# Performance work log

Hardware: AMD Instinct MI355X
Metric: run time of the kernel (lower is better)

The kernel has to match this reference:

```python
import jax, jax.numpy as jnp
import numpy as np

B, S, D, H, L, MLP, WIN = 4, 1024, 256, 8, 2, 1024, 64
HD = D // H
NEG = -1e9  # emulates -inf additive mask; exp underflows to exact 0

_idx = jnp.arange(S)
BAND = jnp.where(jnp.abs(_idx[:, None] - _idx[None, :]) <= WIN, 0.0, NEG).astype(jnp.float32)


def setup_inputs() -> dict:
    key = jax.random.key(0)
    ks = iter(jax.random.split(key, 16))
    r = lambda shape, s=0.02: jax.random.normal(next(ks), shape, dtype=jnp.float32) * s
    return {
        "x": jax.random.normal(next(ks), (B, S, D), dtype=jnp.float32),
        "scale": jnp.ones((1,), jnp.float32) * (D ** -0.5),
        "Win_a": r((L, 3 * D, D)), "bin_a": jnp.zeros((L, 3 * D), jnp.float32),
        "Wout_a": r((L, D, D)), "bout_a": jnp.zeros((L, D), jnp.float32),
        "Win_e": r((L, 3 * D, D)), "bin_e": jnp.zeros((L, 3 * D), jnp.float32),
        "Wout_e": r((L, D, D)), "bout_e": jnp.zeros((L, D), jnp.float32),
        "ln1_g": jnp.ones((L, D), jnp.float32), "ln1_b": jnp.zeros((L, D), jnp.float32),
        "ln2_g": jnp.ones((L, D), jnp.float32), "ln2_b": jnp.zeros((L, D), jnp.float32),
        "W1": r((L, MLP, D)), "b1": jnp.zeros((L, MLP), jnp.float32),
        "W2": r((L, D, MLP)), "b2": jnp.zeros((L, D), jnp.float32),
        "lnf_g": jnp.ones((D,), jnp.float32), "lnf_b": jnp.zeros((D,), jnp.float32),
    }


def _layernorm(x, g, b, eps=1e-5):
    m = jnp.mean(x, axis=-1, keepdims=True)
    v = jnp.mean(jnp.square(x - m), axis=-1, keepdims=True)
    return (x - m) * jax.lax.rsqrt(v + eps) * g + b


def _mha(x, Win, bin_, Wout, bout, mask=None):
    # torch nn.MultiheadAttention (batch_first=True), dropout=0
    b, s, _ = x.shape
    qkv = x @ Win.T + bin_                       # (b, s, 3D)
    q, k, v = jnp.split(qkv, 3, axis=-1)
    split = lambda t: t.reshape(b, s, H, HD).transpose(0, 2, 1, 3)  # (b, H, s, HD)
    q, k, v = split(q), split(k), split(v)
    scores = jnp.einsum('bhqd,bhkd->bhqk', q, k) / np.float32(np.sqrt(HD))
    if mask is not None:
        scores = scores + mask
    attn = jax.nn.softmax(scores, axis=-1)
    out = jnp.einsum('bhqk,bhkd->bhqd', attn, v).transpose(0, 2, 1, 3).reshape(b, s, D)
    return out @ Wout.T + bout


def reference(x, scale, Win_a, bin_a, Wout_a, bout_a, Win_e, bin_e, Wout_e, bout_e,
              ln1_g, ln1_b, ln2_g, ln2_b, W1, b1, W2, b2, lnf_g, lnf_b):
    # ScaledSinusoidalPositionalEncoding returns arange(S)*scale, shape (S,1)
    pos = jnp.arange(S, dtype=jnp.float32) * scale[0]   # (S,)
    x = x + pos[:, None]                                 # broadcast (B,S,D)+(S,1)
    for l in range(L):
        xi = _mha(x, Win_a[l], bin_a[l], Wout_a[l], bout_a[l])
        x = _layernorm(x + xi, ln1_g[l], ln1_b[l])
        xe = _mha(x, Win_e[l], bin_e[l], Wout_e[l], bout_e[l], mask=BAND)
        attended = _layernorm(x + xe, ln2_g[l], ln2_b[l])
        h = jax.nn.gelu(attended @ W1[l].T + b1[l], approximate=False)
        x = attended + h @ W2[l].T + b2[l]
    return _layernorm(x, lnf_g, lnf_b)
```

## Files before the change

kernel.cpp:

```cpp
#include <hip/hip_runtime.h>
#include <math.h>

#define BB 4
#define SS 1024
#define DD 256
#define HH 8
#define HD 32
#define D3 768
#define MLP 1024
#define NTOK (BB * SS)
#define NSEG 4

typedef __attribute__((ext_vector_type(8))) short short8;
typedef __attribute__((ext_vector_type(4))) float f32x4;

__device__ __forceinline__ unsigned short f2bfu(float f) {
    union { float f; unsigned i; } u; u.f = f;
    unsigned r = u.i + 0x7fffu + ((u.i >> 16) & 1u);
    return (unsigned short)(r >> 16);
}
__device__ __forceinline__ float bfu2f(unsigned short h) {
    union { unsigned i; float f; } u; u.i = ((unsigned)h) << 16; return u.f;
}

#define W_TOT 2097152
#define WL0   196608
#define WBLK  (W_TOT / 256)
#define PBLK  (NTOK * DD / 256)
__global__ __launch_bounds__(256) void prep_kernel(
    const float* __restrict__ a0, const float* __restrict__ a1,
    const float* __restrict__ a2, const float* __restrict__ a3,
    const float* __restrict__ a4, const float* __restrict__ a5,
    unsigned short* __restrict__ out, unsigned short* __restrict__ out_lo,
    const float* __restrict__ x, const float* __restrict__ scale,
    float* __restrict__ xf, unsigned short* __restrict__ xh,
    unsigned short* __restrict__ xl)
{
    if (blockIdx.x < WBLK) {
        int i = blockIdx.x * 256 + threadIdx.x;
        const float* s; int off;
        if      (i <  393216) { s = a0; off = 0;       }
        else if (i <  524288) { s = a1; off = 393216;  }
        else if (i <  917504) { s = a2; off = 524288;  }
        else if (i < 1048576) { s = a3; off = 917504;  }
        else if (i < 1572864) { s = a4; off = 1048576; }
        else                  { s = a5; off = 1572864; }
        float v = s[i - off];
        unsigned short h = f2bfu(v);
        out[i] = h;
        if (i < WL0) out_lo[i] = f2bfu(v - bfu2f(h));
    } else {
        int i = (blockIdx.x - WBLK) * 256 + threadIdx.x;
        int s = (i >> 8) & (SS - 1);
        float v = x[i] + (float)s * scale[0];
        xf[i] = v;
        unsigned short h = f2bfu(v);
        xh[i] = h;
        xl[i] = f2bfu(v - bfu2f(h));
    }
}

__device__ __forceinline__ size_t vt_index(int row, int col512) {
    int b = row >> 10, s = row & (SS - 1);
    int h = col512 >> 5, d = col512 & (HD - 1);
    return (((size_t)b * HH + h) * HD + d) * SS + s;
}

#define LDP 40
__global__ __launch_bounds__(256) void gemm_mfma(
    const unsigned short* __restrict__ A, const unsigned short* __restrict__ W,
    const float* __restrict__ bias, const float* __restrict__ resid,
    float* __restrict__ outf, unsigned short* __restrict__ outb,
    unsigned short* __restrict__ vth,
    int M, int N, int K, int act)
{
    __shared__ __align__(16) unsigned short As[64 * LDP];
    __shared__ __align__(16) unsigned short Bs[128 * LDP];
    const int t = threadIdx.x;
    const int lane = t & 63, wave = t >> 6;
    const int wr = wave >> 1, wc = wave & 1;
    const int m0 = blockIdx.y * 64, n0 = blockIdx.x * 128;
    const int sr = t >> 2;
    const int sc = (t & 3) * 8;

    const unsigned short* Ag = A + (size_t)(m0 + sr) * K + sc;
    const unsigned short* Wg = W + (size_t)(n0 + sr) * K + sc;

    f32x4 acc[2][4];
    #pragma unroll
    for (int i = 0; i < 2; i++)
        #pragma unroll
        for (int j = 0; j < 4; j++)
            acc[i][j] = (f32x4){0.f, 0.f, 0.f, 0.f};

    const int lm = lane & 15, lk = (lane >> 4) * 8;

    uint4 a0 = *(const uint4*)(Ag);
    uint4 b0 = *(const uint4*)(Wg);
    uint4 b1 = *(const uint4*)(Wg + (size_t)64 * K);

    for (int k0 = 0; k0 < K; k0 += 32) {
        __syncthreads();
        *(uint4*)&As[sr * LDP + sc]        = a0;
        *(uint4*)&Bs[sr * LDP + sc]        = b0;
        *(uint4*)&Bs[(sr + 64) * LDP + sc] = b1;
        __syncthreads();
        if (k0 + 32 < K) {
            a0 = *(const uint4*)(Ag + k0 + 32);
            b0 = *(const uint4*)(Wg + k0 + 32);
            b1 = *(const uint4*)(Wg + (size_t)64 * K + k0 + 32);
        }

        short8 af[2], bf[4];
        #pragma unroll
        for (int i = 0; i < 2; i++)
            af[i] = *(const short8*)&As[(wr * 32 + i * 16 + lm) * LDP + lk];
        #pragma unroll
        for (int j = 0; j < 4; j++)
            bf[j] = *(const short8*)&Bs[(wc * 64 + j * 16 + lm) * LDP + lk];
        #pragma unroll
        for (int i = 0; i < 2; i++)
            #pragma unroll
            for (int j = 0; j < 4; j++)
                acc[i][j] = __builtin_amdgcn_mfma_f32_16x16x32_bf16(
                    af[i], bf[j], acc[i][j], 0, 0, 0);
    }

    const int lq = lane >> 4;
    #pragma unroll
    for (int j = 0; j < 4; j++) {
        int col = n0 + wc * 64 + j * 16 + lm;
        float bv = bias[col];
        #pragma unroll
        for (int i = 0; i < 2; i++) {
            #pragma unroll
            for (int r = 0; r < 4; r++) {
                int row = m0 + wr * 32 + i * 16 + lq * 4 + r;
                float v = acc[i][j][r] + bv;
                if (act) v = 0.5f * v * (1.0f + erff(v * 0.70710678118654752f));
                if (vth && col >= 2 * DD) {
                    vth[vt_index(row, col - 2 * DD)] = f2bfu(v);
                } else {
                    size_t idx = (size_t)row * N + col;
                    if (resid) v += resid[idx];
                    if (outf) outf[idx] = v;
                    if (outb) outb[idx] = f2bfu(v);
                }
            }
        }
    }
}

template<bool COMBINE, bool DOLN>
__global__ __launch_bounds__(256) void gemm_ln(
    const unsigned short* __restrict__ A,
    const float* __restrict__ Of, const float2* __restrict__ Ml,
    const unsigned short* __restrict__ W, const float* __restrict__ bias,
    const float* __restrict__ resid,
    const float* __restrict__ g, const float* __restrict__ bt,
    float* __restrict__ outf, unsigned short* __restrict__ outb, int K)
{
    __shared__ __align__(16) unsigned short As[16 * LDP];
    __shared__ __align__(16) unsigned short Bs[256 * LDP];
    __shared__ float rsum[4][16];
    __shared__ float rsum2[4][16];
    const int t = threadIdx.x;
    const int lane = t & 63, wave = t >> 6;
    const int m0 = blockIdx.x * 16;
    const int sr = t >> 2;
    const int sc = (t & 3) * 8;
    const int arow = t >> 2;
    const int acol = (t & 3) * 8;

    const unsigned short* Wg = W + (size_t)sr * K + sc;

    f32x4 acc[4];
    #pragma unroll
    for (int j = 0; j < 4; j++) acc[j] = (f32x4){0.f, 0.f, 0.f, 0.f};

    const int lm = lane & 15, lk = (lane >> 4) * 8;
    const int quad = lane >> 4;

    for (int k0 = 0; k0 < K; k0 += 32) {
        unsigned short ab[8];
        const bool aload = (t < 64);
        if (aload) {
            const int token = m0 + arow;
            if (COMBINE) {
                const int h = (k0 + acol) >> 5;
                float2 ml[NSEG];
                float M = -1e30f;
                #pragma unroll
                for (int s = 0; s < NSEG; s++) {
                    ml[s] = Ml[((size_t)s * NTOK + token) * HH + h];
                    M = fmaxf(M, ml[s].x);
                }
                float wgt[NSEG]; float denom = 0.f;
                #pragma unroll
                for (int s = 0; s < NSEG; s++) {
                    wgt[s] = __expf(ml[s].x - M);
                    denom += ml[s].y * wgt[s];
                }
                const float inv = 1.0f / denom;
                float a8[8] = {};
                #pragma unroll
                for (int s = 0; s < NSEG; s++) {
                    const float* p = Of + ((size_t)s * NTOK + token) * DD + k0 + acol;
                    float4 x0 = *(const float4*)p;
                    float4 x1 = *(const float4*)(p + 4);
                    a8[0] += x0.x * wgt[s]; a8[1] += x0.y * wgt[s];
                    a8[2] += x0.z * wgt[s]; a8[3] += x0.w * wgt[s];
                    a8[4] += x1.x * wgt[s]; a8[5] += x1.y * wgt[s];
                    a8[6] += x1.z * wgt[s]; a8[7] += x1.w * wgt[s];
                }
                #pragma unroll
                for (int c = 0; c < 8; c++) ab[c] = f2bfu(a8[c] * inv);
            } else {
                uint4 av = *(const uint4*)(A + (size_t)(m0 + arow) * K + k0 + acol);
                *(uint4*)ab = av;
            }
        }
        uint4 b0 = *(const uint4*)(Wg + k0);
        uint4 b1 = *(const uint4*)(Wg + (size_t)64 * K + k0);
        uint4 b2 = *(const uint4*)(Wg + (size_t)128 * K + k0);
        uint4 b3 = *(const uint4*)(Wg + (size_t)192 * K + k0);
        __syncthreads();
        if (aload) *(uint4*)&As[arow * LDP + acol] = *(uint4*)ab;
        *(uint4*)&Bs[sr * LDP + sc]         = b0;
        *(uint4*)&Bs[(sr + 64) * LDP + sc]  = b1;
        *(uint4*)&Bs[(sr + 128) * LDP + sc] = b2;
        *(uint4*)&Bs[(sr + 192) * LDP + sc] = b3;
        __syncthreads();

        short8 af = *(const short8*)&As[lm * LDP + lk];
        #pragma unroll
        for (int j = 0; j < 4; j++) {
            short8 bf = *(const short8*)&Bs[(wave * 64 + j * 16 + lm) * LDP + lk];
            acc[j] = __builtin_amdgcn_mfma_f32_16x16x32_bf16(af, bf, acc[j], 0, 0, 0);
        }
    }

    #pragma unroll
    for (int j = 0; j < 4; j++) {
        int col = wave * 64 + j * 16 + lm;
        float bv = bias[col];
        #pragma unroll
        for (int r = 0; r < 4; r++) {
            int row = m0 + quad * 4 + r;
            acc[j][r] += bv + resid[(size_t)row * DD + col];
        }
    }
    if (!DOLN) {
        #pragma unroll
        for (int j = 0; j < 4; j++) {
            int col = wave * 64 + j * 16 + lm;
            #pragma unroll
            for (int r = 0; r < 4; r++) {
                int row = m0 + quad * 4 + r;
                size_t idx = (size_t)row * DD + col;
                if (outf) outf[idx] = acc[j][r];
                if (outb) outb[idx] = f2bfu(acc[j][r]);
            }
        }
        return;
    }
    #pragma unroll
    for (int r = 0; r < 4; r++) {
        float s = 0.f;
        #pragma unroll
        for (int j = 0; j < 4; j++) s += acc[j][r];
        s += __shfl_xor(s, 1, 64); s += __shfl_xor(s, 2, 64);
        s += __shfl_xor(s, 4, 64); s += __shfl_xor(s, 8, 64);
        if (lm == 0) rsum[wave][quad * 4 + r] = s;
    }
    __syncthreads();
    float mean_[4];
    #pragma unroll
    for (int r = 0; r < 4; r++) {
        int ri = quad * 4 + r;
        mean_[r] = (rsum[0][ri] + rsum[1][ri] + rsum[2][ri] + rsum[3][ri])
                 * (1.0f / 256.0f);
    }
    #pragma unroll
    for (int r = 0; r < 4; r++) {
        float s2 = 0.f;
        #pragma unroll
        for (int j = 0; j < 4; j++) {
            float d = acc[j][r] - mean_[r];
            s2 += d * d;
        }
        s2 += __shfl_xor(s2, 1, 64); s2 += __shfl_xor(s2, 2, 64);
        s2 += __shfl_xor(s2, 4, 64); s2 += __shfl_xor(s2, 8, 64);
        if (lm == 0) rsum2[wave][quad * 4 + r] = s2;
    }
    __syncthreads();
    float rstd[4];
    #pragma unroll
    for (int r = 0; r < 4; r++) {
        int ri = quad * 4 + r;
        rstd[r] = rsqrtf((rsum2[0][ri] + rsum2[1][ri] + rsum2[2][ri] + rsum2[3][ri])
                         * (1.0f / 256.0f) + 1e-5f);
    }
    #pragma unroll
    for (int j = 0; j < 4; j++) {
        int col = wave * 64 + j * 16 + lm;
        float gv = g[col], bv2 = bt[col];
        #pragma unroll
        for (int r = 0; r < 4; r++) {
            int row = m0 + quad * 4 + r;
            float ov = (acc[j][r] - mean_[r]) * rstd[r] * gv + bv2;
            size_t idx = (size_t)row * DD + col;
            if (outf) outf[idx] = ov;
            if (outb) outb[idx] = f2bfu(ov);
        }
    }
}

__global__ __launch_bounds__(256) void gemm_mfma_split(
    const unsigned short* __restrict__ Ah, const unsigned short* __restrict__ Al,
    const unsigned short* __restrict__ Wh, const unsigned short* __restrict__ Wl,
    const float* __restrict__ bias,
    unsigned short* __restrict__ outh, unsigned short* __restrict__ outl,
    unsigned short* __restrict__ vth,
    int M, int N, int K)
{
    __shared__ __align__(16) unsigned short Ash[64 * LDP];
    __shared__ __align__(16) unsigned short Asl[64 * LDP];
    __shared__ __align__(16) unsigned short Bsh[128 * LDP];
    __shared__ __align__(16) unsigned short Bsl[128 * LDP];
    const int t = threadIdx.x;
    const int lane = t & 63, wave = t >> 6;
    const int wr = wave >> 1, wc = wave & 1;
    const int m0 = blockIdx.y * 64, n0 = blockIdx.x * 128;
    const int sr = t >> 2;
    const int sc = (t & 3) * 8;

    const size_t oA = (size_t)(m0 + sr) * K + sc;
    const size_t oW = (size_t)(n0 + sr) * K + sc;

    f32x4 acc[2][4];
    #pragma unroll
    for (int i = 0; i < 2; i++)
        #pragma unroll
        for (int j = 0; j < 4; j++)
            acc[i][j] = (f32x4){0.f, 0.f, 0.f, 0.f};

    const int lm = lane & 15, lk = (lane >> 4) * 8;

    uint4 ah0 = *(const uint4*)(Ah + oA);
    uint4 al0 = *(const uint4*)(Al + oA);
    uint4 bh0 = *(const uint4*)(Wh + oW);
    uint4 bh1 = *(const uint4*)(Wh + oW + (size_t)64 * K);
    uint4 bl0 = *(const uint4*)(Wl + oW);
    uint4 bl1 = *(const uint4*)(Wl + oW + (size_t)64 * K);

    for (int k0 = 0; k0 < K; k0 += 32) {
        __syncthreads();
        *(uint4*)&Ash[sr * LDP + sc]        = ah0;
        *(uint4*)&Asl[sr * LDP + sc]        = al0;
        *(uint4*)&Bsh[sr * LDP + sc]        = bh0;
        *(uint4*)&Bsh[(sr + 64) * LDP + sc] = bh1;
        *(uint4*)&Bsl[sr * LDP + sc]        = bl0;
        *(uint4*)&Bsl[(sr + 64) * LDP + sc] = bl1;
        __syncthreads();
        if (k0 + 32 < K) {
            ah0 = *(const uint4*)(Ah + oA + k0 + 32);
            al0 = *(const uint4*)(Al + oA + k0 + 32);
            bh0 = *(const uint4*)(Wh + oW + k0 + 32);
            bh1 = *(const uint4*)(Wh + oW + (size_t)64 * K + k0 + 32);
            bl0 = *(const uint4*)(Wl + oW + k0 + 32);
            bl1 = *(const uint4*)(Wl + oW + (size_t)64 * K + k0 + 32);
        }

        short8 afh[2], afl[2], bfh[4], bfl[4];
        #pragma unroll
        for (int i = 0; i < 2; i++) {
            afh[i] = *(const short8*)&Ash[(wr * 32 + i * 16 + lm) * LDP + lk];
            afl[i] = *(const short8*)&Asl[(wr * 32 + i * 16 + lm) * LDP + lk];
        }
        #pragma unroll
        for (int j = 0; j < 4; j++) {
            bfh[j] = *(const short8*)&Bsh[(wc * 64 + j * 16 + lm) * LDP + lk];
            bfl[j] = *(const short8*)&Bsl[(wc * 64 + j * 16 + lm) * LDP + lk];
        }
        #pragma unroll
        for (int i = 0; i < 2; i++)
            #pragma unroll
            for (int j = 0; j < 4; j++) {
                acc[i][j] = __builtin_amdgcn_mfma_f32_16x16x32_bf16(
                    afl[i], bfh[j], acc[i][j], 0, 0, 0);
                acc[i][j] = __builtin_amdgcn_mfma_f32_16x16x32_bf16(
                    afh[i], bfl[j], acc[i][j], 0, 0, 0);
                acc[i][j] = __builtin_amdgcn_mfma_f32_16x16x32_bf16(
                    afh[i], bfh[j], acc[i][j], 0, 0, 0);
            }
    }

    const int lq = lane >> 4;
    #pragma unroll
    for (int j = 0; j < 4; j++) {
        int col = n0 + wc * 64 + j * 16 + lm;
        float bv = bias[col];
        #pragma unroll
        for (int i = 0; i < 2; i++) {
            #pragma unroll
            for (int r = 0; r < 4; r++) {
                int row = m0 + wr * 32 + i * 16 + lq * 4 + r;
                float v = acc[i][j][r] + bv;
                unsigned short h = f2bfu(v);
                if (col >= 2 * DD) {
                    vth[vt_index(row, col - 2 * DD)] = h;
                } else {
                    size_t idx = (size_t)row * N + col;
                    outh[idx] = h;
                    outl[idx] = f2bfu(v - bfu2f(h));
                }
            }
        }
    }
}

__global__ __launch_bounds__(256) void attn_split(
    const unsigned short* __restrict__ qkvh,
    const unsigned short* __restrict__ qkvl,
    const unsigned short* __restrict__ vth,
    float* __restrict__ Of, float2* __restrict__ Ml)
{
    __shared__ __align__(16) unsigned short Ks [64 * 40];
    __shared__ __align__(16) unsigned short Vt [32 * 72];
    __shared__ __align__(16) unsigned short Ps [64 * 72];
    __shared__ __align__(16) unsigned short Ksl[64 * 40];

    const int t = threadIdx.x;
    const int wave = t >> 6, lane = t & 63;
    const int lm = lane & 15, quad = lane >> 4;
    const int i0 = blockIdx.x * 64, h = blockIdx.y;
    const int z = blockIdx.z;
    const int b = z >> 2, seg = z & (NSEG - 1);
    const int sr = t >> 2, sc8 = (t & 3) * 8;
    const int vd = t >> 3, vs8 = (t & 7) * 8;

    const size_t qoff = ((size_t)(b * SS) + i0 + 16 * wave + lm) * D3 + h * HD + quad * 8;
    short8 qh = *(const short8*)(qkvh + qoff);
    short8 ql = *(const short8*)(qkvl + qoff);

    const unsigned short* Kg  = qkvh + (size_t)(b * SS) * D3 + DD + h * HD;
    const unsigned short* Klg = qkvl + (size_t)(b * SS) * D3 + DD + h * HD;
    const unsigned short* Vg  = vth + ((size_t)b * HH + h) * HD * SS;

    float m[4], l[4];
    f32x4 o[2];
    #pragma unroll
    for (int r = 0; r < 4; r++) { m[r] = -1e30f; l[r] = 0.f; }
    o[0] = (f32x4){0.f, 0.f, 0.f, 0.f};
    o[1] = (f32x4){0.f, 0.f, 0.f, 0.f};

    const int per = (SS / 64) / NSEG;
    const int s0 = seg * per, s1 = s0 + per - 1;
    const float scl = 0.17677669529663688f;

    short8 kreg  = *(const short8*)(Kg  + (size_t)(s0 * 64 + sr) * D3 + sc8);
    short8 kregl = *(const short8*)(Klg + (size_t)(s0 * 64 + sr) * D3 + sc8);
    short8 vreg  = *(const short8*)(Vg  + (size_t)vd * SS + s0 * 64 + vs8);

    for (int kt = s0; kt <= s1; kt++) {
        const int k0 = kt * 64;
        __syncthreads();
        *(short8*)&Ks [sr * 40 + sc8] = kreg;
        *(short8*)&Ksl[sr * 40 + sc8] = kregl;
        *(short8*)&Vt [vd * 72 + vs8] = vreg;
        __syncthreads();
        if (kt < s1) {
            kreg  = *(const short8*)(Kg  + (size_t)(k0 + 64 + sr) * D3 + sc8);
            kregl = *(const short8*)(Klg + (size_t)(k0 + 64 + sr) * D3 + sc8);
            vreg  = *(const short8*)(Vg  + (size_t)vd * SS + k0 + 64 + vs8);
        }

        f32x4 s[4];
        #pragma unroll
        for (int cb = 0; cb < 4; cb++) {
            short8 kf  = *(const short8*)&Ks [(16 * cb + lm) * 40 + quad * 8];
            short8 kfl = *(const short8*)&Ksl[(16 * cb + lm) * 40 + quad * 8];
            f32x4 a = (f32x4){0.f, 0.f, 0.f, 0.f};
            a = __builtin_amdgcn_mfma_f32_16x16x32_bf16(ql, kf,  a, 0, 0, 0);
            a = __builtin_amdgcn_mfma_f32_16x16x32_bf16(qh, kfl, a, 0, 0, 0);
            a = __builtin_amdgcn_mfma_f32_16x16x32_bf16(qh, kf,  a, 0, 0, 0);
            s[cb] = a;
        }

        #pragma unroll
        for (int r = 0; r < 4; r++) {
            float s0r = s[0][r] * scl, s1r = s[1][r] * scl;
            float s2r = s[2][r] * scl, s3r = s[3][r] * scl;
            float tm = fmaxf(fmaxf(s0r, s1r), fmaxf(s2r, s3r));
            tm = fmaxf(tm, __shfl_xor(tm, 1, 64));
            tm = fmaxf(tm, __shfl_xor(tm, 2, 64));
            tm = fmaxf(tm, __shfl_xor(tm, 4, 64));
            tm = fmaxf(tm, __shfl_xor(tm, 8, 64));
            float mn = fmaxf(m[r], tm);
            float alpha = __expf(m[r] - mn);
            float p0 = __expf(s0r - mn), p1 = __expf(s1r - mn);
            float p2 = __expf(s2r - mn), p3 = __expf(s3r - mn);
            float ps = p0 + p1 + p2 + p3;
            ps += __shfl_xor(ps, 1, 64);
            ps += __shfl_xor(ps, 2, 64);
            ps += __shfl_xor(ps, 4, 64);
            ps += __shfl_xor(ps, 8, 64);
            l[r] = l[r] * alpha + ps;
            o[0][r] *= alpha;
            o[1][r] *= alpha;
            m[r] = mn;
            const int pr = (16 * wave + quad * 4 + r) * 72 + lm;
            Ps[pr +  0] = f2bfu(p0);
            Ps[pr + 16] = f2bfu(p1);
            Ps[pr + 32] = f2bfu(p2);
            Ps[pr + 48] = f2bfu(p3);
        }

        #pragma unroll
        for (int kc = 0; kc < 2; kc++) {
            short8 pf = *(const short8*)&Ps[(16 * wave + lm) * 72 + 32 * kc + quad * 8];
            #pragma unroll
            for (int nh = 0; nh < 2; nh++) {
                short8 vf = *(const short8*)&Vt[(16 * nh + lm) * 72 + 32 * kc + quad * 8];
                o[nh] = __builtin_amdgcn_mfma_f32_16x16x32_bf16(pf, vf, o[nh], 0, 0, 0);
            }
        }
    }

    #pragma unroll
    for (int r = 0; r < 4; r++) {
        int row = i0 + 16 * wave + quad * 4 + r;
        size_t base = ((size_t)seg * NTOK + b * SS + row) * DD + h * HD + lm;
        Of[base]      = o[0][r];
        Of[base + 16] = o[1][r];
        if (lm == 0)
            Ml[((size_t)seg * NTOK + b * SS + row) * HH + h] =
                make_float2(m[r], l[r]);
    }
}

__global__ __launch_bounds__(256) void attn_fixed(
    const unsigned short* __restrict__ qkvh,
    const unsigned short* __restrict__ vth,
    unsigned short* __restrict__ outb,
    float* __restrict__ Of, float2* __restrict__ Ml,
    int win, int nseg)
{
    __shared__ __align__(16) unsigned short Ks[64 * 40];
    __shared__ __align__(16) unsigned short Vt[32 * 72];
    __shared__ __align__(16) unsigned short Ps[64 * 72];

    const int t = threadIdx.x;
    const int wave = t >> 6, lane = t & 63;
    const int lm = lane & 15, quad = lane >> 4;
    const int i0 = blockIdx.x * 64, h = blockIdx.y;
    const int z = blockIdx.z;
    const int b = z / nseg, seg = z - b * nseg;
    const int sr = t >> 2, sc8 = (t & 3) * 8;
    const int vd = t >> 3, vs8 = (t & 7) * 8;

    const size_t qoff = ((size_t)(b * SS) + i0 + 16 * wave + lm) * D3 + h * HD + quad * 8;
    short8 qh = *(const short8*)(qkvh + qoff);

    const unsigned short* Kg = qkvh + (size_t)(b * SS) * D3 + DD + h * HD;
    const unsigned short* Vg = vth + ((size_t)b * HH + h) * HD * SS;

    float l[4] = {0.f, 0.f, 0.f, 0.f};
    f32x4 o[2];
    o[0] = (f32x4){0.f, 0.f, 0.f, 0.f};
    o[1] = (f32x4){0.f, 0.f, 0.f, 0.f};

    int t0 = 0, t1 = SS / 64 - 1;
    const bool masked = (win < SS);
    if (masked) {
        t0 = (i0 - win) >> 6;        if (t0 < 0) t0 = 0;
        t1 = (i0 + 63 + win) >> 6;   if (t1 > SS / 64 - 1) t1 = SS / 64 - 1;
    }
    const int per = (t1 - t0 + nseg) / nseg;
    const int s0 = t0 + seg * per;
    const int s1 = (s0 + per - 1 < t1) ? (s0 + per - 1) : t1;
    const float scl = 0.17677669529663688f;
    const float M0 = 32.0f;

    short8 kreg = *(const short8*)(Kg + (size_t)(s0 * 64 + sr) * D3 + sc8);
    short8 vreg = *(const short8*)(Vg + (size_t)vd * SS + s0 * 64 + vs8);

    for (int kt = s0; kt <= s1; kt++) {
        const int k0 = kt * 64;
        __syncthreads();
        *(short8*)&Ks[sr * 40 + sc8] = kreg;
        *(short8*)&Vt[vd * 72 + vs8] = vreg;
        __syncthreads();
        if (kt < s1) {
            kreg = *(const short8*)(Kg + (size_t)(k0 + 64 + sr) * D3 + sc8);
            vreg = *(const short8*)(Vg + (size_t)vd * SS + k0 + 64 + vs8);
        }

        f32x4 s[4];
        #pragma unroll
        for (int cb = 0; cb < 4; cb++) {
            short8 kf = *(const short8*)&Ks[(16 * cb + lm) * 40 + quad * 8];
            f32x4 a = (f32x4){0.f, 0.f, 0.f, 0.f};
            a = __builtin_amdgcn_mfma_f32_16x16x32_bf16(qh, kf, a, 0, 0, 0);
            s[cb] = a;
        }

        #pragma unroll
        for (int r = 0; r < 4; r++) {
            float p[4];
            #pragma unroll
            for (int cb = 0; cb < 4; cb++) {
                float v = s[cb][r] * scl;
                if (masked) {
                    int di = (i0 + 16 * wave + quad * 4 + r) - (k0 + 16 * cb + lm);
                    if (di > win || di < -win) v = -1e30f;
                }
                p[cb] = __expf(v - M0);
            }
            l[r] += p[0] + p[1] + p[2] + p[3];
            const int pr = (16 * wave + quad * 4 + r) * 72 + lm;
            Ps[pr +  0] = f2bfu(p[0]);
            Ps[pr + 16] = f2bfu(p[1]);
            Ps[pr + 32] = f2bfu(p[2]);
            Ps[pr + 48] = f2bfu(p[3]);
        }

        #pragma unroll
        for (int kc = 0; kc < 2; kc++) {
            short8 pf = *(const short8*)&Ps[(16 * wave + lm) * 72 + 32 * kc + quad * 8];
            #pragma unroll
            for (int nh = 0; nh < 2; nh++) {
                short8 vf = *(const short8*)&Vt[(16 * nh + lm) * 72 + 32 * kc + quad * 8];
                o[nh] = __builtin_amdgcn_mfma_f32_16x16x32_bf16(pf, vf, o[nh], 0, 0, 0);
            }
        }
    }

    #pragma unroll
    for (int r = 0; r < 4; r++) {
        l[r] += __shfl_xor(l[r], 1, 64);
        l[r] += __shfl_xor(l[r], 2, 64);
        l[r] += __shfl_xor(l[r], 4, 64);
        l[r] += __shfl_xor(l[r], 8, 64);
    }

    if (nseg == 1) {
        #pragma unroll
        for (int r = 0; r < 4; r++) {
            float invl = 1.0f / l[r];
            size_t base = ((size_t)(b * SS) + i0 + 16 * wave + quad * 4 + r) * DD + h * HD + lm;
            outb[base]      = f2bfu(o[0][r] * invl);
            outb[base + 16] = f2bfu(o[1][r] * invl);
        }
    } else {
        #pragma unroll
        for (int r = 0; r < 4; r++) {
            int row = i0 + 16 * wave + quad * 4 + r;
            size_t base = ((size_t)seg * NTOK + b * SS + row) * DD + h * HD + lm;
            Of[base]      = o[0][r];
            Of[base + 16] = o[1][r];
            if (lm == 0)
                Ml[((size_t)seg * NTOK + b * SS + row) * HH + h] =
                    make_float2(M0, l[r]);
        }
    }
}

extern "C" void kernel_launch(void* const* d_in, const int* in_sizes, int n_in,
                              void* d_out, int out_size, void* d_ws, size_t ws_size,
                              hipStream_t stream)
{
    const float* xin   = (const float*)d_in[0];
    const float* scale = (const float*)d_in[1];
    const float* Win_a = (const float*)d_in[2];
    const float* bin_a = (const float*)d_in[3];
    const float* Wout_a= (const float*)d_in[4];
    const float* bout_a= (const float*)d_in[5];
    const float* Win_e = (const float*)d_in[6];
    const float* bin_e = (const float*)d_in[7];
    const float* Wout_e= (const float*)d_in[8];
    const float* bout_e= (const float*)d_in[9];
    const float* ln1_g = (const float*)d_in[10];
    const float* ln1_b = (const float*)d_in[11];
    const float* ln2_g = (const float*)d_in[12];
    const float* ln2_b = (const float*)d_in[13];
    const float* W1    = (const float*)d_in[14];
    const float* b1    = (const float*)d_in[15];
    const float* W2    = (const float*)d_in[16];
    const float* b2    = (const float*)d_in[17];
    const float* lnf_g = (const float*)d_in[18];
    const float* lnf_b = (const float*)d_in[19];

    char* ws = (char*)d_ws;
    float* X    = (float*)ws;                     ws += (size_t)NTOK * DD * 4;
    float* X2   = (float*)ws;                     ws += (size_t)NTOK * DD * 4;
    unsigned short* Xb   = (unsigned short*)ws;   ws += (size_t)NTOK * DD * 2;
    unsigned short* Xlb  = (unsigned short*)ws;   ws += (size_t)NTOK * DD * 2;
    unsigned short* X2b  = (unsigned short*)ws;   ws += (size_t)NTOK * DD * 2;
    unsigned short* ATb  = (unsigned short*)ws;   ws += (size_t)NTOK * DD * 2;
    unsigned short* QKVb = (unsigned short*)ws;   ws += (size_t)NTOK * D3 * 2;
    unsigned short* QKVl = (unsigned short*)ws;   ws += (size_t)NTOK * D3 * 2;
    unsigned short* VTh  = (unsigned short*)ws;   ws += (size_t)NTOK * DD * 2;
    unsigned short* HMLb = (unsigned short*)ws;   ws += (size_t)NTOK * MLP * 2;
    unsigned short* Wb   = (unsigned short*)ws;   ws += (size_t)W_TOT * 2;
    unsigned short* Wl0  = (unsigned short*)ws;   ws += (size_t)WL0 * 2;
    float2* Ml           = (float2*)ws;           ws += (size_t)NSEG * NTOK * HH * 8;
    float* Of            = (float*)ws;            ws += (size_t)NSEG * NTOK * DD * 4;

    unsigned short* WinA_b  = Wb + 0;
    unsigned short* WoutA_b = Wb + 393216;
    unsigned short* WinE_b  = Wb + 524288;
    unsigned short* WoutE_b = Wb + 917504;
    unsigned short* W1_b    = Wb + 1048576;
    unsigned short* W2_b    = Wb + 1572864;

    prep_kernel<<<WBLK + PBLK, 256, 0, stream>>>(
        Win_a, Wout_a, Win_e, Wout_e, W1, W2, Wb, Wl0,
        xin, scale, X, Xb, Xlb);

    float* cur = X;            float* oth = X2;
    unsigned short* curb = Xb; unsigned short* othb = X2b;

    for (int l = 0; l < 2; l++) {
        if (l == 0) {
            gemm_mfma_split<<<dim3(D3 / 128, NTOK / 64), 256, 0, stream>>>(
                Xb, Xlb, WinA_b, Wl0, bin_a, QKVb, QKVl, VTh, NTOK, D3, DD);
            attn_split<<<dim3(SS / 64, HH, BB * NSEG), 256, 0, stream>>>(
                QKVb, QKVl, VTh, Of, Ml);
        } else {
            gemm_mfma<<<dim3(D3 / 128, NTOK / 64), 256, 0, stream>>>(
                curb, WinA_b + (size_t)l * D3 * DD, bin_a + (size_t)l * D3,
                nullptr, nullptr, QKVb, VTh, NTOK, D3, DD, 0);
            attn_fixed<<<dim3(SS / 64, HH, BB * NSEG), 256, 0, stream>>>(
                QKVb, VTh, nullptr, Of, Ml, 1 << 28, NSEG);
        }
        gemm_ln<true, true><<<NTOK / 16, 256, 0, stream>>>(
            nullptr, Of, Ml, WoutA_b + (size_t)l * DD * DD,
            bout_a + (size_t)l * DD, cur,
            ln1_g + l * DD, ln1_b + l * DD, oth, othb, DD);

        gemm_mfma<<<dim3(D3 / 128, NTOK / 64), 256, 0, stream>>>(
            othb, WinE_b + (size_t)l * D3 * DD, bin_e + (size_t)l * D3,
            nullptr, nullptr, QKVb, VTh, NTOK, D3, DD, 0);
        attn_fixed<<<dim3(SS / 64, HH, BB), 256, 0, stream>>>(
            QKVb, VTh, ATb, nullptr, nullptr, 64, 1);
        gemm_ln<false, true><<<NTOK / 16, 256, 0, stream>>>(
            ATb, nullptr, nullptr, WoutE_b + (size_t)l * DD * DD,
            bout_e + (size_t)l * DD, oth,
            ln2_g + l * DD, ln2_b + l * DD, cur, curb, DD);

        gemm_mfma<<<dim3(MLP / 128, NTOK / 64), 256, 0, stream>>>(
            curb, W1_b + (size_t)l * MLP * DD, b1 + (size_t)l * MLP,
            nullptr, nullptr, HMLb, nullptr, NTOK, MLP, DD, 1);
        if (l == 0) {
            gemm_ln<false, false><<<NTOK / 16, 256, 0, stream>>>(
                HMLb, nullptr, nullptr, W2_b + (size_t)l * DD * MLP,
                b2 + (size_t)l * DD, cur,
                nullptr, nullptr, oth, othb, MLP);
            float* tf = cur; cur = oth; oth = tf;
            unsigned short* tb = curb; curb = othb; othb = tb;
        } else {
            gemm_ln<false, true><<<NTOK / 16, 256, 0, stream>>>(
                HMLb, nullptr, nullptr, W2_b + (size_t)l * DD * MLP,
                b2 + (size_t)l * DD, cur,
                lnf_g, lnf_b, (float*)d_out, nullptr, MLP);
        }
    }
}
```

Measured before the change: 329.7 us.

## Stage full A tile in LDS once and stream W fragments directly into registers

The gemm_ln kernel now loads the entire 16xK activation tile (or the combined split-attention output) into shared memory in a single pass with one barrier. Weight fragments are read straight from global memory into registers through a four-stage rotating prefetch, so the per-k-step LDS staging of the 256-row weight tile and its two barriers per iteration are removed. K becomes a template parameter so the loop fully unrolls. The cost is more registers, an LDS footprint that grows with K (about 33 KB when K=1024), and uncoalesced strided global reads of W per wave.

```diff
diff --git a/kernel.cpp b/kernel.cpp
--- a/kernel.cpp
+++ b/kernel.cpp
@@ -151,92 +151,98 @@
     }
 }
 
-template<bool COMBINE, bool DOLN>
+template<bool COMBINE, bool DOLN, int K>
 __global__ __launch_bounds__(256) void gemm_ln(
     const unsigned short* __restrict__ A,
     const float* __restrict__ Of, const float2* __restrict__ Ml,
     const unsigned short* __restrict__ W, const float* __restrict__ bias,
     const float* __restrict__ resid,
     const float* __restrict__ g, const float* __restrict__ bt,
-    float* __restrict__ outf, unsigned short* __restrict__ outb, int K)
+    float* __restrict__ outf, unsigned short* __restrict__ outb)
 {
-    __shared__ __align__(16) unsigned short As[16 * LDP];
-    __shared__ __align__(16) unsigned short Bs[256 * LDP];
+    constexpr int LDA = K + 8;
+    constexpr int NS  = K / 32;
+    __shared__ __align__(16) unsigned short As[16 * LDA];
     __shared__ float rsum[4][16];
     __shared__ float rsum2[4][16];
     const int t = threadIdx.x;
     const int lane = t & 63, wave = t >> 6;
     const int m0 = blockIdx.x * 16;
-    const int sr = t >> 2;
-    const int sc = (t & 3) * 8;
-    const int arow = t >> 2;
-    const int acol = (t & 3) * 8;
-
-    const unsigned short* Wg = W + (size_t)sr * K + sc;
+    const int lm = lane & 15, quad = lane >> 4;
+
+    const unsigned short* Wp = W + (size_t)(wave * 64 + lm) * K + quad * 8;
+    short8 bf[4][4];
+    #pragma unroll
+    for (int s = 0; s < 4; s++)
+        #pragma unroll
+        for (int j = 0; j < 4; j++)
+            bf[s][j] = *(const short8*)(Wp + (size_t)(j * 16) * K + s * 32);
+
+    if (COMBINE) {
+        const int row = t >> 4, cg = t & 15;
+        const int token = m0 + row;
+        const int h = cg >> 1;
+        float2 ml[NSEG];
+        float M = -1e30f;
+        #pragma unroll
+        for (int s = 0; s < NSEG; s++) {
+            ml[s] = Ml[((size_t)s * NTOK + token) * HH + h];
+            M = fmaxf(M, ml[s].x);
+        }
+        float wgt[NSEG]; float denom = 0.f;
+        #pragma unroll
+        for (int s = 0; s < NSEG; s++) {
+            wgt[s] = __expf(ml[s].x - M);
+            denom += ml[s].y * wgt[s];
+        }
+        const float inv = 1.0f / denom;
+        float a16[16];
+        #pragma unroll
+        for (int c = 0; c < 16; c++) a16[c] = 0.f;
+        #pragma unroll
+        for (int s = 0; s < NSEG; s++) {
+            const float* p = Of + ((size_t)s * NTOK + token) * DD + cg * 16;
+            #pragma unroll
+            for (int c4 = 0; c4 < 4; c4++) {
+                float4 x = *(const float4*)(p + c4 * 4);
+                a16[c4 * 4 + 0] += x.x * wgt[s];
+                a16[c4 * 4 + 1] += x.y * wgt[s];
+                a16[c4 * 4 + 2] += x.z * wgt[s];
+                a16[c4 * 4 + 3] += x.w * wgt[s];
+            }
+        }
+        __align__(16) unsigned short ab[16];
+        #pragma unroll
+        for (int c = 0; c < 16; c++) ab[c] = f2bfu(a16[c] * inv);
+        *(uint4*)&As[row * LDA + cg * 16]     = *(uint4*)&ab[0];
+        *(uint4*)&As[row * LDA + cg * 16 + 8] = *(uint4*)&ab[8];
+    } else {
+        #pragma unroll
+        for (int u = t; u < 16 * (K / 8); u += 256) {
+            int row = u / (K / 8), cg = u % (K / 8);
+            *(uint4*)&As[row * LDA + cg * 8] =
+                *(const uint4*)(A + (size_t)(m0 + row) * K + cg * 8);
+        }
+    }
+    __syncthreads();
 
     f32x4 acc[4];
     #pragma unroll
     for (int j = 0; j < 4; j++) acc[j] = (f32x4){0.f, 0.f, 0.f, 0.f};
 
-    const int lm = lane & 15, lk = (lane >> 4) * 8;
-    const int quad = lane >> 4;
-
-    for (int k0 = 0; k0 < K; k0 += 32) {
-        unsigned short ab[8];
-        const bool aload = (t < 64);
-        if (aload) {
-            const int token = m0 + arow;
-            if (COMBINE) {
-                const int h = (k0 + acol) >> 5;
-                float2 ml[NSEG];
-                float M = -1e30f;
-                #pragma unroll
-                for (int s = 0; s < NSEG; s++) {
-                    ml[s] = Ml[((size_t)s * NTOK + token) * HH + h];
-                    M = fmaxf(M, ml[s].x);
-                }
-                float wgt[NSEG]; float denom = 0.f;
-                #pragma unroll
-                for (int s = 0; s < NSEG; s++) {
-                    wgt[s] = __expf(ml[s].x - M);
-                    denom += ml[s].y * wgt[s];
-                }
-                const float inv = 1.0f / denom;
-                float a8[8] = {};
-                #pragma unroll
-                for (int s = 0; s < NSEG; s++) {
-                    const float* p = Of + ((size_t)s * NTOK + token) * DD + k0 + acol;
-                    float4 x0 = *(const float4*)p;
-                    float4 x1 = *(const float4*)(p + 4);
-                    a8[0] += x0.x * wgt[s]; a8[1] += x0.y * wgt[s];
-                    a8[2] += x0.z * wgt[s]; a8[3] += x0.w * wgt[s];
-                    a8[4] += x1.x * wgt[s]; a8[5] += x1.y * wgt[s];
-                    a8[6] += x1.z * wgt[s]; a8[7] += x1.w * wgt[s];
-                }
-                #pragma unroll
-                for (int c = 0; c < 8; c++) ab[c] = f2bfu(a8[c] * inv);
-            } else {
-                uint4 av = *(const uint4*)(A + (size_t)(m0 + arow) * K + k0 + acol);
-                *(uint4*)ab = av;
-            }
-        }
-        uint4 b0 = *(const uint4*)(Wg + k0);
-        uint4 b1 = *(const uint4*)(Wg + (size_t)64 * K + k0);
-        uint4 b2 = *(const uint4*)(Wg + (size_t)128 * K + k0);
-        uint4 b3 = *(const uint4*)(Wg + (size_t)192 * K + k0);
-        __syncthreads();
-        if (aload) *(uint4*)&As[arow * LDP + acol] = *(uint4*)ab;
-        *(uint4*)&Bs[sr * LDP + sc]         = b0;
-        *(uint4*)&Bs[(sr + 64) * LDP + sc]  = b1;
-        *(uint4*)&Bs[(sr + 128) * LDP + sc] = b2;
-        *(uint4*)&Bs[(sr + 192) * LDP + sc] = b3;
-        __syncthreads();
-
-        short8 af = *(const short8*)&As[lm * LDP + lk];
-        #pragma unroll
-        for (int j = 0; j < 4; j++) {
-            short8 bf = *(const short8*)&Bs[(wave * 64 + j * 16 + lm) * LDP + lk];
-            acc[j] = __builtin_amdgcn_mfma_f32_16x16x32_bf16(af, bf, acc[j], 0, 0, 0);
+    #pragma unroll
+    for (int k = 0; k < NS; k++) {
+        const int r4 = k & 3;
+        short8 af = *(const short8*)&As[lm * LDA + k * 32 + quad * 8];
+        #pragma unroll
+        for (int j = 0; j < 4; j++)
+            acc[j] = __builtin_amdgcn_mfma_f32_16x16x32_bf16(
+                af, bf[r4][j], acc[j], 0, 0, 0);
+        if (k + 4 < NS) {
+            #pragma unroll
+            for (int j = 0; j < 4; j++)
+                bf[r4][j] = *(const short8*)(Wp + (size_t)(j * 16) * K
+                                             + (k + 4) * 32);
         }
     }
 
@@ -735,36 +741,36 @@
             attn_fixed<<<dim3(SS / 64, HH, BB * NSEG), 256, 0, stream>>>(
                 QKVb, VTh, nullptr, Of, Ml, 1 << 28, NSEG);
         }
-        gemm_ln<true, true><<<NTOK / 16, 256, 0, stream>>>(
+        gemm_ln<true, true, DD><<<NTOK / 16, 256, 0, stream>>>(
             nullptr, Of, Ml, WoutA_b + (size_t)l * DD * DD,
             bout_a + (size_t)l * DD, cur,
-            ln1_g + l * DD, ln1_b + l * DD, oth, othb, DD);
+            ln1_g + l * DD, ln1_b + l * DD, oth, othb);
 
         gemm_mfma<<<dim3(D3 / 128, NTOK / 64), 256, 0, stream>>>(
             othb, WinE_b + (size_t)l * D3 * DD, bin_e + (size_t)l * D3,
             nullptr, nullptr, QKVb, VTh, NTOK, D3, DD, 0);
         attn_fixed<<<dim3(SS / 64, HH, BB), 256, 0, stream>>>(
             QKVb, VTh, ATb, nullptr, nullptr, 64, 1);
-        gemm_ln<false, true><<<NTOK / 16, 256, 0, stream>>>(
+        gemm_ln<false, true, DD><<<NTOK / 16, 256, 0, stream>>>(
             ATb, nullptr, nullptr, WoutE_b + (size_t)l * DD * DD,
             bout_e + (size_t)l * DD, oth,
-            ln2_g + l * DD, ln2_b + l * DD, cur, curb, DD);
+            ln2_g + l * DD, ln2_b + l * DD, cur, curb);
 
         gemm_mfma<<<dim3(MLP / 128, NTOK / 64), 256, 0, stream>>>(
             curb, W1_b + (size_t)l * MLP * DD, b1 + (size_t)l * MLP,
             nullptr, nullptr, HMLb, nullptr, NTOK, MLP, DD, 1);
         if (l == 0) {
-            gemm_ln<false, false><<<NTOK / 16, 256, 0, stream>>>(
+            gemm_ln<false, false, MLP><<<NTOK / 16, 256, 0, stream>>>(
                 HMLb, nullptr, nullptr, W2_b + (size_t)l * DD * MLP,
                 b2 + (size_t)l * DD, cur,
-                nullptr, nullptr, oth, othb, MLP);
+                nullptr, nullptr, oth, othb);
             float* tf = cur; cur = oth; oth = tf;
             unsigned short* tb = curb; curb = othb; othb = tb;
         } else {
-            gemm_ln<false, true><<<NTOK / 16, 256, 0, stream>>>(
+            gemm_ln<false, true, MLP><<<NTOK / 16, 256, 0, stream>>>(
                 HMLb, nullptr, nullptr, W2_b + (size_t)l * DD * MLP,
                 b2 + (size_t)l * DD, cur,
-                lnf_g, lnf_b, (float*)d_out, nullptr, MLP);
-        }
-    }
-}
+                lnf_g, lnf_b, (float*)d_out, nullptr);
+        }
+    }
+}
```

Result: faster. 317.8 us (median of 2 runs) (-3.6%).
